# Kernel optimization log

Measured on AMD Instinct MI355X. Metric: run time of the kernel, lower is better.

The kernel has to match this reference:

```python
import jax, jax.numpy as jnp
import numpy as np


def setup_inputs() -> dict:
    key = jax.random.key(0)
    ks = jax.random.split(key, 6)
    B, S, H, I, E = 2, 1024, 1024, 2816, 8
    W = 0.02  # weight init scale
    return {
        "x": jax.random.normal(ks[0], (B, S, H), jnp.float32),
        "w_router": jax.random.normal(ks[1], (H, E), jnp.float32) * W,
        "w_gate": jax.random.normal(ks[2], (E, H, I), jnp.float32) * W,
        "w_up": jax.random.normal(ks[3], (E, H, I), jnp.float32) * W,
        "w_down": jax.random.normal(ks[4], (E, I, H), jnp.float32) * W,
        "b_down": jnp.zeros((E, H), jnp.float32),
    }


def reference(x, w_router, w_gate, w_up, w_down, b_down):
    # Eval path of PrunedLlamaSMoEBlock: noiseless router, top-k select, softmax
    # over selected logits, SwiGLU experts, scatter-add combine.
    NUM_SELECTS = 2
    T = x.shape[0] * x.shape[1]
    E = w_router.shape[1]
    flat_x = x.reshape(T, -1)                      # [T,H]

    logits = flat_x @ w_router                     # [T,E]
    top_vals, top_idx = jax.lax.top_k(logits, NUM_SELECTS)   # [T,k]
    gw = jax.nn.softmax(top_vals.astype(jnp.float32), axis=1).astype(x.dtype)

    # Dense combine weights: combine[t,e] = sum_k gw[t,k] * (top_idx[t,k]==e)
    combine = jnp.zeros((T, E), x.dtype).at[
        jnp.arange(T)[:, None], top_idx
    ].add(gw)                                      # [T,E]

    # SwiGLU experts over all tokens (weighted by combine, zero if unselected)
    g = jnp.einsum("th,ehi->tei", flat_x, w_gate)  # [T,E,I]
    u = jnp.einsum("th,ehi->tei", flat_x, w_up)    # [T,E,I]
    a = jax.nn.silu(g) * u                         # [T,E,I]
    y = jnp.einsum("tei,eih->teh", a, w_down) + b_down[None]  # [T,E,H]

    out = jnp.einsum("te,teh->th", combine, y)     # [T,H]
    return out.reshape(x.shape)
```

## Files before the change

kernel.cpp:

```cpp
#include <hip/hip_runtime.h>
#include <math.h>

#define HD __device__ __forceinline__

constexpr int TT = 2048;
constexpr int HH = 1024;
constexpr int II = 2816;
constexpr int EE = 8;
constexpr int NK1 = HH / 64;
constexpr int NK2 = II / 64;
constexpr int KS2 = 2;
constexpr int HALF2 = NK2 / KS2;
constexpr int MAXTILES = 40;
constexpr int NSLOT = 2 * TT;

typedef short  bf16x8  __attribute__((ext_vector_type(8)));
typedef float  floatx4 __attribute__((ext_vector_type(4)));
typedef unsigned short ushortx8 __attribute__((ext_vector_type(8)));

constexpr size_t OFF_XB    = 0;
constexpr size_t OFF_WGT   = OFF_XB    + (size_t)TT*HH*2;
constexpr size_t OFF_WUT   = OFF_WGT   + (size_t)EE*II*HH*2;
constexpr size_t OFF_WDT   = OFF_WUT   + (size_t)EE*II*HH*2;
constexpr size_t OFF_ABUF  = OFF_WDT   + (size_t)EE*HH*II*2;
constexpr size_t OFF_CNT   = OFF_ABUF  + (size_t)2*TT*II*2;
constexpr size_t OFF_OFFS  = OFF_CNT   + 256;
constexpr size_t OFF_MDESC = OFF_OFFS  + 256;
constexpr size_t OFF_EMETA = OFF_MDESC + 256;
constexpr size_t OFF_WMETA = OFF_EMETA + 16384;
constexpr size_t OFF_TLIST = OFF_WMETA + 16384;
constexpr size_t OFF_SLOT  = OFF_TLIST + 16384;
constexpr size_t OFF_YBUF  = OFF_WGT;

HD unsigned short f2bf(float f) {
  union { float f; unsigned int u; } v; v.f = f;
  return (unsigned short)((v.u + 0x7fffu + ((v.u >> 16) & 1u)) >> 16);
}

HD void load_lds16(const void* gptr, void* lptr) {
  __builtin_amdgcn_global_load_lds(
      (const __attribute__((address_space(1))) void*)gptr,
      (__attribute__((address_space(3))) void*)lptr,
      16, 0, 0);
}

__global__ __launch_bounds__(256)
void prep_router_kernel(const float* __restrict__ x, const float* __restrict__ w_router,
                        unsigned short* __restrict__ xb,
                        int* __restrict__ emeta, float* __restrict__ wmeta) {
  const int wave = threadIdx.x >> 6;
  const int lane = threadIdx.x & 63;
  const int t = blockIdx.x * 4 + wave;
  const float* xr = x + (size_t)t * HH;
  unsigned short* xo = xb + (size_t)t * HH;

  float acc[EE];
#pragma unroll
  for (int e = 0; e < EE; ++e) acc[e] = 0.f;

#pragma unroll
  for (int it = 0; it < 4; ++it) {
    const int h0 = it * 256 + lane * 4;
    const floatx4 v = __builtin_nontemporal_load((const floatx4*)(xr + h0));
    ushort4 o;
    o.x = f2bf(v[0]); o.y = f2bf(v[1]); o.z = f2bf(v[2]); o.w = f2bf(v[3]);
    *(ushort4*)(xo + h0) = o;
    const float vv[4] = {v[0], v[1], v[2], v[3]};
#pragma unroll
    for (int j = 0; j < 4; ++j) {
      const float* wr = w_router + (size_t)(h0 + j) * EE;
      const float4 w0 = ((const float4*)wr)[0];
      const float4 w1 = ((const float4*)wr)[1];
      acc[0] += vv[j] * w0.x; acc[1] += vv[j] * w0.y;
      acc[2] += vv[j] * w0.z; acc[3] += vv[j] * w0.w;
      acc[4] += vv[j] * w1.x; acc[5] += vv[j] * w1.y;
      acc[6] += vv[j] * w1.z; acc[7] += vv[j] * w1.w;
    }
  }
#pragma unroll
  for (int e = 0; e < EE; ++e) {
#pragma unroll
    for (int off = 32; off > 0; off >>= 1) acc[e] += __shfl_xor(acc[e], off, 64);
  }
  if (lane == 0) {
    int e0 = 0; float v0 = acc[0];
#pragma unroll
    for (int e = 1; e < EE; ++e) if (acc[e] > v0) { v0 = acc[e]; e0 = e; }
    int e1 = -1; float v1 = -3.4e38f;
#pragma unroll
    for (int e = 0; e < EE; ++e) if (e != e0 && acc[e] > v1) { v1 = acc[e]; e1 = e; }
    const float ex = __expf(v1 - v0);
    const float s  = 1.f + ex;
    emeta[2 * t] = e0; emeta[2 * t + 1] = e1;
    wmeta[2 * t] = 1.f / s; wmeta[2 * t + 1] = ex / s;
  }
}

__global__ __launch_bounds__(256)
void transpose_one_kernel(const float* __restrict__ src, unsigned short* __restrict__ dst,
                          int R, int C, int nct) {
  const int e = blockIdx.y;
  const int rt = blockIdx.x / nct;
  const int ct = blockIdx.x % nct;
  const size_t base = (size_t)e * R * C;
  const int R0 = rt * 64;
  const int C0 = ct * 128;

  const int lane = threadIdx.x & 63;
  const int wave = threadIdx.x >> 6;
  const int r0 = R0 + (lane & 7) * 8;
  const int c0 = C0 + wave * 32 + (lane >> 3) * 4;

  floatx4 v[8];
  const float* sp = src + base + (size_t)r0 * C + c0;
#pragma unroll
  for (int j = 0; j < 8; ++j)
    v[j] = __builtin_nontemporal_load((const floatx4*)(sp + (size_t)j * C));

  unsigned short* dp = dst + base + (size_t)c0 * R + r0;
#pragma unroll
  for (int jj = 0; jj < 4; ++jj) {
    ushortx8 o;
#pragma unroll
    for (int j = 0; j < 8; ++j) o[j] = f2bf(v[j][jj]);
    *(ushortx8*)(dp + (size_t)jj * R) = o;
  }
}

__global__ __launch_bounds__(256)
void scanfill_kernel(const int* __restrict__ emeta,
                     int* __restrict__ offsets, int* __restrict__ mdesc,
                     int* __restrict__ token_list, int* __restrict__ slotmap) {
  __shared__ int s_tot[EE];
  __shared__ int s_scan[256];
  const int e = blockIdx.x;
  const int tid = threadIdx.x;
  constexpr int CH = TT / 256;
  const int t0 = tid * CH;
  int lc[EE];
#pragma unroll
  for (int i = 0; i < EE; ++i) lc[i] = 0;
  int ep[CH][2];
#pragma unroll
  for (int k = 0; k < CH; ++k) {
    const int a = emeta[2 * (t0 + k)];
    const int b = emeta[2 * (t0 + k) + 1];
    ep[k][0] = a; ep[k][1] = b;
#pragma unroll
    for (int i = 0; i < EE; ++i) lc[i] += (a == i) + (b == i);
  }
  if (tid < EE) s_tot[tid] = 0;
  __syncthreads();
#pragma unroll
  for (int i = 0; i < EE; ++i) if (lc[i]) atomicAdd(&s_tot[i], lc[i]);
  int cnt = 0;
#pragma unroll
  for (int i = 0; i < EE; ++i) if (i == e) cnt = lc[i];
  s_scan[tid] = cnt;
  __syncthreads();
  int v = cnt;
  for (int d = 1; d < 256; d <<= 1) {
    const int add = (tid >= d) ? s_scan[tid - d] : 0;
    __syncthreads();
    v += add;
    s_scan[tid] = v;
    __syncthreads();
  }
  int off_e = 0;
#pragma unroll
  for (int i = 0; i < EE; ++i) off_e += (i < e) ? s_tot[i] : 0;
  if (e == 0 && tid == 0) {
    int s = 0, nt = 0;
    for (int i = 0; i < EE; ++i) {
      const int c = s_tot[i];
      offsets[i] = s;
      for (int m = 0; m < c; m += 128) mdesc[1 + nt++] = (i << 20) | m;
      s += c;
    }
    offsets[EE] = s;
    mdesc[0] = nt;
  }
  int pos = off_e + (v - cnt);
#pragma unroll
  for (int k = 0; k < CH; ++k) {
    const int t = t0 + k;
#pragma unroll
    for (int s = 0; s < 2; ++s) {
      if (ep[k][s] == e) {
        token_list[pos] = t;
        slotmap[2 * t + s] = pos;
        ++pos;
      }
    }
  }
}

__global__ __launch_bounds__(256, 4)
void gemm1_kernel(const unsigned short* __restrict__ xb,
                  const unsigned short* __restrict__ wgt,
                  const unsigned short* __restrict__ wut,
                  const int* __restrict__ offsets,
                  const int* __restrict__ mdesc,
                  const int* __restrict__ token_list,
                  unsigned short* __restrict__ Abuf) {
  constexpr int NWG1 = (II / 64) * MAXTILES;
  constexpr int CHUNK1 = NWG1 / 8;
  const int p = (int)(blockIdx.y * gridDim.x + blockIdx.x);
  const int idx = (p & 7) * CHUNK1 + (p >> 3);
  const int bx = idx / MAXTILES;
  const int by = idx % MAXTILES;

  if (by >= mdesc[0]) return;
  const int d = mdesc[1 + by];
  const int e = d >> 20;
  const int m_base = d & 0xFFFFF;
  const int off_e = offsets[e];
  const int n_e = offsets[e + 1] - off_e;
  const int n_base = bx * 64;

  __shared__ __attribute__((aligned(16))) unsigned short ldsA[128 * 64];
  __shared__ __attribute__((aligned(16))) unsigned short ldsG[64 * 64];
  __shared__ __attribute__((aligned(16))) unsigned short ldsU[64 * 64];

  const int tid = threadIdx.x;
  const int wave = tid >> 6;
  const int lane = tid & 63;
  const int quad = lane >> 4;
  const int l16 = lane & 15;
  const int wave_m = (wave & 1) * 64;
  const int wave_n = (wave >> 1) * 32;

  const int srow = lane >> 3;
  const int clog = (lane & 7) ^ srow;

  const unsigned short* gA[4];
  const unsigned short* gG[2];
  const unsigned short* gU[2];
#pragma unroll
  for (int it = 0; it < 4; ++it) {
    const int r = it * 32 + wave * 8 + srow;
    int ar = m_base + r; if (ar > n_e - 1) ar = n_e - 1;
    const int tok = token_list[off_e + ar];
    gA[it] = xb + (size_t)tok * HH + clog * 8;
  }
#pragma unroll
  for (int it = 0; it < 2; ++it) {
    const int r = it * 32 + wave * 8 + srow;
    gG[it] = wgt + ((size_t)e * II + (n_base + r)) * HH + clog * 8;
    gU[it] = wut + ((size_t)e * II + (n_base + r)) * HH + clog * 8;
  }

  floatx4 accG[4][2], accU[4][2];
  const floatx4 fz = {0.f, 0.f, 0.f, 0.f};
#pragma unroll
  for (int i = 0; i < 4; ++i)
#pragma unroll
    for (int j = 0; j < 2; ++j) { accG[i][j] = fz; accU[i][j] = fz; }

  for (int kt = 0; kt < NK1; ++kt) {
    const int k0 = kt * 64;
#pragma unroll
    for (int it = 0; it < 4; ++it)
      load_lds16(gA[it] + k0, &ldsA[(it * 32 + wave * 8) * 64]);
#pragma unroll
    for (int it = 0; it < 2; ++it) {
      load_lds16(gG[it] + k0, &ldsG[(it * 32 + wave * 8) * 64]);
      load_lds16(gU[it] + k0, &ldsU[(it * 32 + wave * 8) * 64]);
    }
    __syncthreads();
#pragma unroll
    for (int ks = 0; ks < 2; ++ks) {
      bf16x8 af[4], bg[2], bu[2];
#pragma unroll
      for (int f = 0; f < 4; ++f) {
        const int rowA = wave_m + f * 16 + l16;
        const int cA = (ks * 4 + quad) ^ (rowA & 7);
        af[f] = *(const bf16x8*)&ldsA[rowA * 64 + cA * 8];
      }
#pragma unroll
      for (int f = 0; f < 2; ++f) {
        const int rowB = wave_n + f * 16 + l16;
        const int cB = (ks * 4 + quad) ^ (rowB & 7);
        bg[f] = *(const bf16x8*)&ldsG[rowB * 64 + cB * 8];
        bu[f] = *(const bf16x8*)&ldsU[rowB * 64 + cB * 8];
      }
#pragma unroll
      for (int mf = 0; mf < 4; ++mf)
#pragma unroll
        for (int nf = 0; nf < 2; ++nf) {
          accG[mf][nf] = __builtin_amdgcn_mfma_f32_16x16x32_bf16(af[mf], bg[nf], accG[mf][nf], 0, 0, 0);
          accU[mf][nf] = __builtin_amdgcn_mfma_f32_16x16x32_bf16(af[mf], bu[nf], accU[mf][nf], 0, 0, 0);
        }
    }
    __syncthreads();
  }

#pragma unroll
  for (int mf = 0; mf < 4; ++mf)
#pragma unroll
    for (int nf = 0; nf < 2; ++nf) {
      const int col = n_base + wave_n + nf * 16 + l16;
#pragma unroll
      for (int j = 0; j < 4; ++j) {
        const int r = m_base + wave_m + mf * 16 + quad * 4 + j;
        if (r < n_e) {
          const float g = accG[mf][nf][j];
          const float u = accU[mf][nf][j];
          const float a = (g / (1.f + __expf(-g))) * u;
          Abuf[(size_t)(off_e + r) * II + col] = f2bf(a);
        }
      }
    }
}

__global__ __launch_bounds__(256, 3)
void gemm2_kernel(const unsigned short* __restrict__ Abuf,
                  const unsigned short* __restrict__ wdt,
                  const int* __restrict__ offsets,
                  const int* __restrict__ mdesc,
                  float* __restrict__ Ybuf) {
  const int p = (int)(blockIdx.x + gridDim.x * (blockIdx.y + gridDim.y * blockIdx.z));
  const int idx = (p & 7) * 80 + (p >> 3);
  const int by = idx % MAXTILES;
  const int g = idx / MAXTILES;
  const int bx = g & 7;
  const int split = g >> 3;

  if (by >= mdesc[0]) return;
  const int d = mdesc[1 + by];
  const int e = d >> 20;
  const int m_base = d & 0xFFFFF;
  const int off_e = offsets[e];
  const int n_e = offsets[e + 1] - off_e;
  const int n_base = bx * 128;
  const int kt_lo = split * HALF2;
  const int kt_hi = kt_lo + HALF2;

  __shared__ __attribute__((aligned(16))) unsigned short ldsA[128 * 64];
  __shared__ __attribute__((aligned(16))) unsigned short ldsB[128 * 64];

  const int tid = threadIdx.x;
  const int wave = tid >> 6;
  const int lane = tid & 63;
  const int quad = lane >> 4;
  const int l16 = lane & 15;
  const int wave_m = (wave & 1) * 64;
  const int wave_n = (wave >> 1) * 64;

  const int srow = lane >> 3;
  const int clog = (lane & 7) ^ srow;

  const unsigned short* gA[4];
  const unsigned short* gB[4];
#pragma unroll
  for (int it = 0; it < 4; ++it) {
    const int r = it * 32 + wave * 8 + srow;
    int ar = m_base + r; if (ar > n_e - 1) ar = n_e - 1;
    gA[it] = Abuf + (size_t)(off_e + ar) * II + clog * 8;
  }
#pragma unroll
  for (int it = 0; it < 4; ++it) {
    const int r = it * 32 + wave * 8 + srow;
    gB[it] = wdt + ((size_t)e * HH + (n_base + r)) * II + clog * 8;
  }

  floatx4 acc[4][4];
  const floatx4 fz = {0.f, 0.f, 0.f, 0.f};
#pragma unroll
  for (int i = 0; i < 4; ++i)
#pragma unroll
    for (int j = 0; j < 4; ++j) acc[i][j] = fz;

  for (int kt = kt_lo; kt < kt_hi; ++kt) {
    const int k0 = kt * 64;
#pragma unroll
    for (int it = 0; it < 4; ++it)
      load_lds16(gA[it] + k0, &ldsA[(it * 32 + wave * 8) * 64]);
#pragma unroll
    for (int it = 0; it < 4; ++it)
      load_lds16(gB[it] + k0, &ldsB[(it * 32 + wave * 8) * 64]);
    __syncthreads();
#pragma unroll
    for (int ks = 0; ks < 2; ++ks) {
      bf16x8 af[4], bf[4];
#pragma unroll
      for (int f = 0; f < 4; ++f) {
        const int rowA = wave_m + f * 16 + l16;
        const int cA = (ks * 4 + quad) ^ (rowA & 7);
        af[f] = *(const bf16x8*)&ldsA[rowA * 64 + cA * 8];
      }
#pragma unroll
      for (int f = 0; f < 4; ++f) {
        const int rowB = wave_n + f * 16 + l16;
        const int cB = (ks * 4 + quad) ^ (rowB & 7);
        bf[f] = *(const bf16x8*)&ldsB[rowB * 64 + cB * 8];
      }
#pragma unroll
      for (int mf = 0; mf < 4; ++mf)
#pragma unroll
        for (int nf = 0; nf < 4; ++nf)
          acc[mf][nf] = __builtin_amdgcn_mfma_f32_16x16x32_bf16(af[mf], bf[nf], acc[mf][nf], 0, 0, 0);
    }
    __syncthreads();
  }

  float* yb = Ybuf + (size_t)split * NSLOT * HH;
#pragma unroll
  for (int mf = 0; mf < 4; ++mf)
#pragma unroll
    for (int nf = 0; nf < 4; ++nf) {
      const int col = n_base + wave_n + nf * 16 + l16;
#pragma unroll
      for (int j = 0; j < 4; ++j) {
        const int r = m_base + wave_m + mf * 16 + quad * 4 + j;
        if (r < n_e)
          yb[(size_t)(off_e + r) * HH + col] = acc[mf][nf][j];
      }
    }
}

__global__ __launch_bounds__(256)
void combine_kernel(const float* __restrict__ Ybuf, const int* __restrict__ slotmap,
                    const int* __restrict__ emeta, const float* __restrict__ wmeta,
                    const float* __restrict__ b_down, float* __restrict__ out) {
  const int t = blockIdx.x;
  const int c = threadIdx.x;
  const int s0 = slotmap[2 * t], s1 = slotmap[2 * t + 1];
  const int e0 = emeta[2 * t], e1 = emeta[2 * t + 1];
  const float g0 = wmeta[2 * t], g1 = wmeta[2 * t + 1];
  const floatx4 y00 = __builtin_nontemporal_load((const floatx4*)(Ybuf + (size_t)s0 * HH) + c);
  const floatx4 y01 = __builtin_nontemporal_load((const floatx4*)(Ybuf + ((size_t)NSLOT + s0) * HH) + c);
  const floatx4 y10 = __builtin_nontemporal_load((const floatx4*)(Ybuf + (size_t)s1 * HH) + c);
  const floatx4 y11 = __builtin_nontemporal_load((const floatx4*)(Ybuf + ((size_t)NSLOT + s1) * HH) + c);
  const float4 b0 = ((const float4*)(b_down + (size_t)e0 * HH))[c];
  const float4 b1 = ((const float4*)(b_down + (size_t)e1 * HH))[c];
  float4 o;
  o.x = g0 * (y00[0] + y01[0] + b0.x) + g1 * (y10[0] + y11[0] + b1.x);
  o.y = g0 * (y00[1] + y01[1] + b0.y) + g1 * (y10[1] + y11[1] + b1.y);
  o.z = g0 * (y00[2] + y01[2] + b0.z) + g1 * (y10[2] + y11[2] + b1.z);
  o.w = g0 * (y00[3] + y01[3] + b0.w) + g1 * (y10[3] + y11[3] + b1.w);
  ((float4*)(out + (size_t)t * HH))[c] = o;
}

extern "C" void kernel_launch(void* const* d_in, const int* in_sizes, int n_in,
                              void* d_out, int out_size, void* d_ws, size_t ws_size,
                              hipStream_t stream) {
  const float* x        = (const float*)d_in[0];
  const float* w_router = (const float*)d_in[1];
  const float* w_gate   = (const float*)d_in[2];
  const float* w_up     = (const float*)d_in[3];
  const float* w_down   = (const float*)d_in[4];
  const float* b_down   = (const float*)d_in[5];
  float* out = (float*)d_out;

  char* ws = (char*)d_ws;
  unsigned short* xb   = (unsigned short*)(ws + OFF_XB);
  unsigned short* wgt  = (unsigned short*)(ws + OFF_WGT);
  unsigned short* wut  = (unsigned short*)(ws + OFF_WUT);
  unsigned short* wdt  = (unsigned short*)(ws + OFF_WDT);
  unsigned short* Abuf = (unsigned short*)(ws + OFF_ABUF);
  int*   offsets = (int*)(ws + OFF_OFFS);
  int*   mdesc   = (int*)(ws + OFF_MDESC);
  int*   emeta   = (int*)(ws + OFF_EMETA);
  float* wmeta   = (float*)(ws + OFF_WMETA);
  int*   tlist   = (int*)(ws + OFF_TLIST);
  int*   slotmap = (int*)(ws + OFF_SLOT);
  float* Ybuf    = (float*)(ws + OFF_YBUF);

  prep_router_kernel<<<TT / 4, 256, 0, stream>>>(x, w_router, xb, emeta, wmeta);
  scanfill_kernel<<<EE, 256, 0, stream>>>(emeta, offsets, mdesc, tlist, slotmap);
  transpose_one_kernel<<<dim3(352, EE), 256, 0, stream>>>(w_gate, wgt, HH, II, II / 128);
  transpose_one_kernel<<<dim3(352, EE), 256, 0, stream>>>(w_up,   wut, HH, II, II / 128);
  transpose_one_kernel<<<dim3(352, EE), 256, 0, stream>>>(w_down, wdt, II, HH, HH / 128);
  gemm1_kernel<<<dim3(II / 64, MAXTILES), 256, 0, stream>>>(xb, wgt, wut, offsets, mdesc, tlist, Abuf);
  gemm2_kernel<<<dim3(HH / 128, MAXTILES, KS2), 256, 0, stream>>>(Abuf, wdt, offsets, mdesc, Ybuf);
  combine_kernel<<<TT, 256, 0, stream>>>(Ybuf, slotmap, emeta, wmeta, b_down, out);
}
```

Before: 392.0 us.

## Merge prologue kernels and fuse combine into gemm2 via atomic scatter-add

Folds the router/convert kernel and the three weight transpose kernels into a single prologue launch, which also zeroes the output. It removes the combine kernel by having gemm2 scale each tile by its gate weight, add the bias on one split, and atomically add into the output rows indexed by the token list. This avoids the fp32 Y buffer round-trip and several launches, in exchange for many scattered fp32 atomics and a summation order that is no longer deterministic.

```diff
diff --git a/kernel.cpp b/kernel.cpp
--- a/kernel.cpp
+++ b/kernel.cpp
@@ -12,7 +12,6 @@
 constexpr int KS2 = 2;
 constexpr int HALF2 = NK2 / KS2;
 constexpr int MAXTILES = 40;
-constexpr int NSLOT = 2 * TT;
 
 typedef short  bf16x8  __attribute__((ext_vector_type(8)));
 typedef float  floatx4 __attribute__((ext_vector_type(4)));
@@ -23,14 +22,12 @@
 constexpr size_t OFF_WUT   = OFF_WGT   + (size_t)EE*II*HH*2;
 constexpr size_t OFF_WDT   = OFF_WUT   + (size_t)EE*II*HH*2;
 constexpr size_t OFF_ABUF  = OFF_WDT   + (size_t)EE*HH*II*2;
-constexpr size_t OFF_CNT   = OFF_ABUF  + (size_t)2*TT*II*2;
-constexpr size_t OFF_OFFS  = OFF_CNT   + 256;
+constexpr size_t OFF_OFFS  = OFF_ABUF  + (size_t)2*TT*II*2;
 constexpr size_t OFF_MDESC = OFF_OFFS  + 256;
 constexpr size_t OFF_EMETA = OFF_MDESC + 256;
 constexpr size_t OFF_WMETA = OFF_EMETA + 16384;
 constexpr size_t OFF_TLIST = OFF_WMETA + 16384;
-constexpr size_t OFF_SLOT  = OFF_TLIST + 16384;
-constexpr size_t OFF_YBUF  = OFF_WGT;
+constexpr size_t OFF_GWL   = OFF_TLIST + 16384;
 
 HD unsigned short f2bf(float f) {
   union { float f; unsigned int u; } v; v.f = f;
@@ -45,63 +42,77 @@
 }
 
 __global__ __launch_bounds__(256)
-void prep_router_kernel(const float* __restrict__ x, const float* __restrict__ w_router,
-                        unsigned short* __restrict__ xb,
-                        int* __restrict__ emeta, float* __restrict__ wmeta) {
-  const int wave = threadIdx.x >> 6;
-  const int lane = threadIdx.x & 63;
-  const int t = blockIdx.x * 4 + wave;
-  const float* xr = x + (size_t)t * HH;
-  unsigned short* xo = xb + (size_t)t * HH;
-
-  float acc[EE];
-#pragma unroll
-  for (int e = 0; e < EE; ++e) acc[e] = 0.f;
-
-#pragma unroll
-  for (int it = 0; it < 4; ++it) {
-    const int h0 = it * 256 + lane * 4;
-    const floatx4 v = __builtin_nontemporal_load((const floatx4*)(xr + h0));
-    ushort4 o;
-    o.x = f2bf(v[0]); o.y = f2bf(v[1]); o.z = f2bf(v[2]); o.w = f2bf(v[3]);
-    *(ushort4*)(xo + h0) = o;
-    const float vv[4] = {v[0], v[1], v[2], v[3]};
-#pragma unroll
-    for (int j = 0; j < 4; ++j) {
-      const float* wr = w_router + (size_t)(h0 + j) * EE;
-      const float4 w0 = ((const float4*)wr)[0];
-      const float4 w1 = ((const float4*)wr)[1];
-      acc[0] += vv[j] * w0.x; acc[1] += vv[j] * w0.y;
-      acc[2] += vv[j] * w0.z; acc[3] += vv[j] * w0.w;
-      acc[4] += vv[j] * w1.x; acc[5] += vv[j] * w1.y;
-      acc[6] += vv[j] * w1.z; acc[7] += vv[j] * w1.w;
-    }
-  }
-#pragma unroll
-  for (int e = 0; e < EE; ++e) {
-#pragma unroll
-    for (int off = 32; off > 0; off >>= 1) acc[e] += __shfl_xor(acc[e], off, 64);
-  }
-  if (lane == 0) {
-    int e0 = 0; float v0 = acc[0];
-#pragma unroll
-    for (int e = 1; e < EE; ++e) if (acc[e] > v0) { v0 = acc[e]; e0 = e; }
-    int e1 = -1; float v1 = -3.4e38f;
-#pragma unroll
-    for (int e = 0; e < EE; ++e) if (e != e0 && acc[e] > v1) { v1 = acc[e]; e1 = e; }
-    const float ex = __expf(v1 - v0);
-    const float s  = 1.f + ex;
-    emeta[2 * t] = e0; emeta[2 * t + 1] = e1;
-    wmeta[2 * t] = 1.f / s; wmeta[2 * t + 1] = ex / s;
-  }
-}
-
-__global__ __launch_bounds__(256)
-void transpose_one_kernel(const float* __restrict__ src, unsigned short* __restrict__ dst,
-                          int R, int C, int nct) {
-  const int e = blockIdx.y;
-  const int rt = blockIdx.x / nct;
-  const int ct = blockIdx.x % nct;
+void prologue_kernel(const float* __restrict__ x, const float* __restrict__ w_router,
+                     const float* __restrict__ wg, const float* __restrict__ wu,
+                     const float* __restrict__ wd,
+                     unsigned short* __restrict__ xb, int* __restrict__ emeta,
+                     float* __restrict__ wmeta, float* __restrict__ out,
+                     unsigned short* __restrict__ wgt, unsigned short* __restrict__ wut,
+                     unsigned short* __restrict__ wdt) {
+  const int ty = blockIdx.y;
+  if (ty == 0) {
+    if ((int)blockIdx.x >= TT / 4) return;
+    const int wave = threadIdx.x >> 6;
+    const int lane = threadIdx.x & 63;
+    const int t = blockIdx.x * 4 + wave;
+    const float* xr = x + (size_t)t * HH;
+    unsigned short* xo = xb + (size_t)t * HH;
+    float* orow = out + (size_t)t * HH;
+
+    float acc[EE];
+#pragma unroll
+    for (int e = 0; e < EE; ++e) acc[e] = 0.f;
+
+#pragma unroll
+    for (int it = 0; it < 4; ++it) {
+      const int h0 = it * 256 + lane * 4;
+      const floatx4 v = __builtin_nontemporal_load((const floatx4*)(xr + h0));
+      ushort4 o;
+      o.x = f2bf(v[0]); o.y = f2bf(v[1]); o.z = f2bf(v[2]); o.w = f2bf(v[3]);
+      *(ushort4*)(xo + h0) = o;
+      const float4 z = {0.f, 0.f, 0.f, 0.f};
+      *(float4*)(orow + h0) = z;
+      const float vv[4] = {v[0], v[1], v[2], v[3]};
+#pragma unroll
+      for (int j = 0; j < 4; ++j) {
+        const float* wr = w_router + (size_t)(h0 + j) * EE;
+        const float4 w0 = ((const float4*)wr)[0];
+        const float4 w1 = ((const float4*)wr)[1];
+        acc[0] += vv[j] * w0.x; acc[1] += vv[j] * w0.y;
+        acc[2] += vv[j] * w0.z; acc[3] += vv[j] * w0.w;
+        acc[4] += vv[j] * w1.x; acc[5] += vv[j] * w1.y;
+        acc[6] += vv[j] * w1.z; acc[7] += vv[j] * w1.w;
+      }
+    }
+#pragma unroll
+    for (int e = 0; e < EE; ++e) {
+#pragma unroll
+      for (int off = 32; off > 0; off >>= 1) acc[e] += __shfl_xor(acc[e], off, 64);
+    }
+    if (lane == 0) {
+      int e0 = 0; float v0 = acc[0];
+#pragma unroll
+      for (int e = 1; e < EE; ++e) if (acc[e] > v0) { v0 = acc[e]; e0 = e; }
+      int e1 = -1; float v1 = -3.4e38f;
+#pragma unroll
+      for (int e = 0; e < EE; ++e) if (e != e0 && acc[e] > v1) { v1 = acc[e]; e1 = e; }
+      const float ex = __expf(v1 - v0);
+      const float s  = 1.f + ex;
+      emeta[2 * t] = e0; emeta[2 * t + 1] = e1;
+      wmeta[2 * t] = 1.f / s; wmeta[2 * t + 1] = ex / s;
+    }
+    return;
+  }
+
+  const float* src; unsigned short* dst; int R, C;
+  if (ty == 1)      { src = wg; dst = wgt; R = HH; C = II; }
+  else if (ty == 2) { src = wu; dst = wut; R = HH; C = II; }
+  else              { src = wd; dst = wdt; R = II; C = HH; }
+  const int e = blockIdx.x / 352;
+  const int tile = blockIdx.x % 352;
+  const int nct = C / 128;
+  const int rt = tile / nct;
+  const int ct = tile % nct;
   const size_t base = (size_t)e * R * C;
   const int R0 = rt * 64;
   const int C0 = ct * 128;
@@ -128,9 +139,9 @@
 }
 
 __global__ __launch_bounds__(256)
-void scanfill_kernel(const int* __restrict__ emeta,
+void scanfill_kernel(const int* __restrict__ emeta, const float* __restrict__ wmeta,
                      int* __restrict__ offsets, int* __restrict__ mdesc,
-                     int* __restrict__ token_list, int* __restrict__ slotmap) {
+                     int* __restrict__ token_list, float* __restrict__ gw_list) {
   __shared__ int s_tot[EE];
   __shared__ int s_scan[256];
   const int e = blockIdx.x;
@@ -188,7 +199,7 @@
     for (int s = 0; s < 2; ++s) {
       if (ep[k][s] == e) {
         token_list[pos] = t;
-        slotmap[2 * t + s] = pos;
+        gw_list[pos] = wmeta[2 * t + s];
         ++pos;
       }
     }
@@ -316,9 +327,12 @@
 __global__ __launch_bounds__(256, 3)
 void gemm2_kernel(const unsigned short* __restrict__ Abuf,
                   const unsigned short* __restrict__ wdt,
+                  const float* __restrict__ b_down,
                   const int* __restrict__ offsets,
                   const int* __restrict__ mdesc,
-                  float* __restrict__ Ybuf) {
+                  const int* __restrict__ token_list,
+                  const float* __restrict__ gw_list,
+                  float* __restrict__ out) {
   const int p = (int)(blockIdx.x + gridDim.x * (blockIdx.y + gridDim.y * blockIdx.z));
   const int idx = (p & 7) * 80 + (p >> 3);
   const int by = idx % MAXTILES;
@@ -404,42 +418,22 @@
     __syncthreads();
   }
 
-  float* yb = Ybuf + (size_t)split * NSLOT * HH;
 #pragma unroll
   for (int mf = 0; mf < 4; ++mf)
 #pragma unroll
     for (int nf = 0; nf < 4; ++nf) {
       const int col = n_base + wave_n + nf * 16 + l16;
+      const float bd = (split == 0) ? b_down[e * HH + col] : 0.f;
 #pragma unroll
       for (int j = 0; j < 4; ++j) {
         const int r = m_base + wave_m + mf * 16 + quad * 4 + j;
-        if (r < n_e)
-          yb[(size_t)(off_e + r) * HH + col] = acc[mf][nf][j];
-      }
-    }
-}
-
-__global__ __launch_bounds__(256)
-void combine_kernel(const float* __restrict__ Ybuf, const int* __restrict__ slotmap,
-                    const int* __restrict__ emeta, const float* __restrict__ wmeta,
-                    const float* __restrict__ b_down, float* __restrict__ out) {
-  const int t = blockIdx.x;
-  const int c = threadIdx.x;
-  const int s0 = slotmap[2 * t], s1 = slotmap[2 * t + 1];
-  const int e0 = emeta[2 * t], e1 = emeta[2 * t + 1];
-  const float g0 = wmeta[2 * t], g1 = wmeta[2 * t + 1];
-  const floatx4 y00 = __builtin_nontemporal_load((const floatx4*)(Ybuf + (size_t)s0 * HH) + c);
-  const floatx4 y01 = __builtin_nontemporal_load((const floatx4*)(Ybuf + ((size_t)NSLOT + s0) * HH) + c);
-  const floatx4 y10 = __builtin_nontemporal_load((const floatx4*)(Ybuf + (size_t)s1 * HH) + c);
-  const floatx4 y11 = __builtin_nontemporal_load((const floatx4*)(Ybuf + ((size_t)NSLOT + s1) * HH) + c);
-  const float4 b0 = ((const float4*)(b_down + (size_t)e0 * HH))[c];
-  const float4 b1 = ((const float4*)(b_down + (size_t)e1 * HH))[c];
-  float4 o;
-  o.x = g0 * (y00[0] + y01[0] + b0.x) + g1 * (y10[0] + y11[0] + b1.x);
-  o.y = g0 * (y00[1] + y01[1] + b0.y) + g1 * (y10[1] + y11[1] + b1.y);
-  o.z = g0 * (y00[2] + y01[2] + b0.z) + g1 * (y10[2] + y11[2] + b1.z);
-  o.w = g0 * (y00[3] + y01[3] + b0.w) + g1 * (y10[3] + y11[3] + b1.w);
-  ((float4*)(out + (size_t)t * HH))[c] = o;
+        if (r < n_e) {
+          const int cr = off_e + r;
+          atomicAdd(&out[(size_t)token_list[cr] * HH + col],
+                    gw_list[cr] * (acc[mf][nf][j] + bd));
+        }
+      }
+    }
 }
 
 extern "C" void kernel_launch(void* const* d_in, const int* in_sizes, int n_in,
@@ -464,15 +458,12 @@
   int*   emeta   = (int*)(ws + OFF_EMETA);
   float* wmeta   = (float*)(ws + OFF_WMETA);
   int*   tlist   = (int*)(ws + OFF_TLIST);
-  int*   slotmap = (int*)(ws + OFF_SLOT);
-  float* Ybuf    = (float*)(ws + OFF_YBUF);
-
-  prep_router_kernel<<<TT / 4, 256, 0, stream>>>(x, w_router, xb, emeta, wmeta);
-  scanfill_kernel<<<EE, 256, 0, stream>>>(emeta, offsets, mdesc, tlist, slotmap);
-  transpose_one_kernel<<<dim3(352, EE), 256, 0, stream>>>(w_gate, wgt, HH, II, II / 128);
-  transpose_one_kernel<<<dim3(352, EE), 256, 0, stream>>>(w_up,   wut, HH, II, II / 128);
-  transpose_one_kernel<<<dim3(352, EE), 256, 0, stream>>>(w_down, wdt, II, HH, HH / 128);
+  float* gwl     = (float*)(ws + OFF_GWL);
+
+  prologue_kernel<<<dim3(352 * EE, 4), 256, 0, stream>>>(
+      x, w_router, w_gate, w_up, w_down, xb, emeta, wmeta, out, wgt, wut, wdt);
+  scanfill_kernel<<<EE, 256, 0, stream>>>(emeta, wmeta, offsets, mdesc, tlist, gwl);
   gemm1_kernel<<<dim3(II / 64, MAXTILES), 256, 0, stream>>>(xb, wgt, wut, offsets, mdesc, tlist, Abuf);
-  gemm2_kernel<<<dim3(HH / 128, MAXTILES, KS2), 256, 0, stream>>>(Abuf, wdt, offsets, mdesc, Ybuf);
-  combine_kernel<<<TT, 256, 0, stream>>>(Ybuf, slotmap, emeta, wmeta, b_down, out);
-}
+  gemm2_kernel<<<dim3(HH / 128, MAXTILES, KS2), 256, 0, stream>>>(
+      Abuf, wdt, b_down, offsets, mdesc, tlist, gwl, out);
+}
```

New measurement: 407.3 us. +3.9%, slower.

## Fuse router prep and three weight transposes into one prologue kernel

Applied to the files above, without the earlier changes.

Merges the router/bf16-cast kernel and the three weight transpose-and-convert launches into a single prologue kernel that uses grid y to select the job. This removes three launches and lets the router work overlap with the transposes. The transpose tile changes from 64x128 to 32x256, so each lane now reads wider contiguous rows. Gemm1's launch bounds go from 4 to 5 waves per SIMD, which could limit registers and cause spills. An unused workspace offset is also dropped.

```diff
diff --git a/kernel.cpp b/kernel.cpp
--- a/kernel.cpp
+++ b/kernel.cpp
@@ -23,8 +23,7 @@
 constexpr size_t OFF_WUT   = OFF_WGT   + (size_t)EE*II*HH*2;
 constexpr size_t OFF_WDT   = OFF_WUT   + (size_t)EE*II*HH*2;
 constexpr size_t OFF_ABUF  = OFF_WDT   + (size_t)EE*HH*II*2;
-constexpr size_t OFF_CNT   = OFF_ABUF  + (size_t)2*TT*II*2;
-constexpr size_t OFF_OFFS  = OFF_CNT   + 256;
+constexpr size_t OFF_OFFS  = OFF_ABUF  + (size_t)2*TT*II*2;
 constexpr size_t OFF_MDESC = OFF_OFFS  + 256;
 constexpr size_t OFF_EMETA = OFF_MDESC + 256;
 constexpr size_t OFF_WMETA = OFF_EMETA + 16384;
@@ -45,71 +44,83 @@
 }
 
 __global__ __launch_bounds__(256)
-void prep_router_kernel(const float* __restrict__ x, const float* __restrict__ w_router,
-                        unsigned short* __restrict__ xb,
-                        int* __restrict__ emeta, float* __restrict__ wmeta) {
-  const int wave = threadIdx.x >> 6;
-  const int lane = threadIdx.x & 63;
-  const int t = blockIdx.x * 4 + wave;
-  const float* xr = x + (size_t)t * HH;
-  unsigned short* xo = xb + (size_t)t * HH;
-
-  float acc[EE];
-#pragma unroll
-  for (int e = 0; e < EE; ++e) acc[e] = 0.f;
-
-#pragma unroll
-  for (int it = 0; it < 4; ++it) {
-    const int h0 = it * 256 + lane * 4;
-    const floatx4 v = __builtin_nontemporal_load((const floatx4*)(xr + h0));
-    ushort4 o;
-    o.x = f2bf(v[0]); o.y = f2bf(v[1]); o.z = f2bf(v[2]); o.w = f2bf(v[3]);
-    *(ushort4*)(xo + h0) = o;
-    const float vv[4] = {v[0], v[1], v[2], v[3]};
-#pragma unroll
-    for (int j = 0; j < 4; ++j) {
-      const float* wr = w_router + (size_t)(h0 + j) * EE;
-      const float4 w0 = ((const float4*)wr)[0];
-      const float4 w1 = ((const float4*)wr)[1];
-      acc[0] += vv[j] * w0.x; acc[1] += vv[j] * w0.y;
-      acc[2] += vv[j] * w0.z; acc[3] += vv[j] * w0.w;
-      acc[4] += vv[j] * w1.x; acc[5] += vv[j] * w1.y;
-      acc[6] += vv[j] * w1.z; acc[7] += vv[j] * w1.w;
-    }
-  }
-#pragma unroll
-  for (int e = 0; e < EE; ++e) {
-#pragma unroll
-    for (int off = 32; off > 0; off >>= 1) acc[e] += __shfl_xor(acc[e], off, 64);
-  }
-  if (lane == 0) {
-    int e0 = 0; float v0 = acc[0];
-#pragma unroll
-    for (int e = 1; e < EE; ++e) if (acc[e] > v0) { v0 = acc[e]; e0 = e; }
-    int e1 = -1; float v1 = -3.4e38f;
-#pragma unroll
-    for (int e = 0; e < EE; ++e) if (e != e0 && acc[e] > v1) { v1 = acc[e]; e1 = e; }
-    const float ex = __expf(v1 - v0);
-    const float s  = 1.f + ex;
-    emeta[2 * t] = e0; emeta[2 * t + 1] = e1;
-    wmeta[2 * t] = 1.f / s; wmeta[2 * t + 1] = ex / s;
-  }
-}
-
-__global__ __launch_bounds__(256)
-void transpose_one_kernel(const float* __restrict__ src, unsigned short* __restrict__ dst,
-                          int R, int C, int nct) {
-  const int e = blockIdx.y;
-  const int rt = blockIdx.x / nct;
-  const int ct = blockIdx.x % nct;
+void prologue_kernel(const float* __restrict__ x, const float* __restrict__ w_router,
+                     const float* __restrict__ wg, const float* __restrict__ wu,
+                     const float* __restrict__ wd,
+                     unsigned short* __restrict__ xb, int* __restrict__ emeta,
+                     float* __restrict__ wmeta,
+                     unsigned short* __restrict__ wgt, unsigned short* __restrict__ wut,
+                     unsigned short* __restrict__ wdt) {
+  const int ty = blockIdx.y;
+  if (ty == 0) {
+    if ((int)blockIdx.x >= TT / 4) return;
+    const int wave = threadIdx.x >> 6;
+    const int lane = threadIdx.x & 63;
+    const int t = blockIdx.x * 4 + wave;
+    const float* xr = x + (size_t)t * HH;
+    unsigned short* xo = xb + (size_t)t * HH;
+
+    float acc[EE];
+#pragma unroll
+    for (int e = 0; e < EE; ++e) acc[e] = 0.f;
+
+#pragma unroll
+    for (int it = 0; it < 4; ++it) {
+      const int h0 = it * 256 + lane * 4;
+      const floatx4 v = __builtin_nontemporal_load((const floatx4*)(xr + h0));
+      ushort4 o;
+      o.x = f2bf(v[0]); o.y = f2bf(v[1]); o.z = f2bf(v[2]); o.w = f2bf(v[3]);
+      *(ushort4*)(xo + h0) = o;
+      const float vv[4] = {v[0], v[1], v[2], v[3]};
+#pragma unroll
+      for (int j = 0; j < 4; ++j) {
+        const float* wr = w_router + (size_t)(h0 + j) * EE;
+        const float4 w0 = ((const float4*)wr)[0];
+        const float4 w1 = ((const float4*)wr)[1];
+        acc[0] += vv[j] * w0.x; acc[1] += vv[j] * w0.y;
+        acc[2] += vv[j] * w0.z; acc[3] += vv[j] * w0.w;
+        acc[4] += vv[j] * w1.x; acc[5] += vv[j] * w1.y;
+        acc[6] += vv[j] * w1.z; acc[7] += vv[j] * w1.w;
+      }
+    }
+#pragma unroll
+    for (int e = 0; e < EE; ++e) {
+#pragma unroll
+      for (int off = 32; off > 0; off >>= 1) acc[e] += __shfl_xor(acc[e], off, 64);
+    }
+    if (lane == 0) {
+      int e0 = 0; float v0 = acc[0];
+#pragma unroll
+      for (int e = 1; e < EE; ++e) if (acc[e] > v0) { v0 = acc[e]; e0 = e; }
+      int e1 = -1; float v1 = -3.4e38f;
+#pragma unroll
+      for (int e = 0; e < EE; ++e) if (e != e0 && acc[e] > v1) { v1 = acc[e]; e1 = e; }
+      const float ex = __expf(v1 - v0);
+      const float s  = 1.f + ex;
+      emeta[2 * t] = e0; emeta[2 * t + 1] = e1;
+      wmeta[2 * t] = 1.f / s; wmeta[2 * t + 1] = ex / s;
+    }
+    return;
+  }
+
+  const float* src; unsigned short* dst; int R, C, nct;
+  if (ty == 1)      { src = wg; dst = wgt; R = HH; C = II; nct = II / 256; }
+  else if (ty == 2) { src = wu; dst = wut; R = HH; C = II; nct = II / 256; }
+  else              { src = wd; dst = wdt; R = II; C = HH; nct = HH / 256; }
+  const int e = blockIdx.x / 352;
+  const int tile = blockIdx.x % 352;
+  const int rt = tile / nct;
+  const int ct = tile % nct;
   const size_t base = (size_t)e * R * C;
-  const int R0 = rt * 64;
-  const int C0 = ct * 128;
+  const int R0 = rt * 32;
+  const int C0 = ct * 256;
 
   const int lane = threadIdx.x & 63;
   const int wave = threadIdx.x >> 6;
-  const int r0 = R0 + (lane & 7) * 8;
-  const int c0 = C0 + wave * 32 + (lane >> 3) * 4;
+  const int rowgrp = lane >> 4;
+  const int colchunk = lane & 15;
+  const int r0 = R0 + rowgrp * 8;
+  const int c0 = C0 + wave * 64 + colchunk * 4;
 
   floatx4 v[8];
   const float* sp = src + base + (size_t)r0 * C + c0;
@@ -195,7 +206,7 @@
   }
 }
 
-__global__ __launch_bounds__(256, 4)
+__global__ __launch_bounds__(256, 5)
 void gemm1_kernel(const unsigned short* __restrict__ xb,
                   const unsigned short* __restrict__ wgt,
                   const unsigned short* __restrict__ wut,
@@ -467,11 +478,9 @@
   int*   slotmap = (int*)(ws + OFF_SLOT);
   float* Ybuf    = (float*)(ws + OFF_YBUF);
 
-  prep_router_kernel<<<TT / 4, 256, 0, stream>>>(x, w_router, xb, emeta, wmeta);
+  prologue_kernel<<<dim3(352 * EE, 4), 256, 0, stream>>>(
+      x, w_router, w_gate, w_up, w_down, xb, emeta, wmeta, wgt, wut, wdt);
   scanfill_kernel<<<EE, 256, 0, stream>>>(emeta, offsets, mdesc, tlist, slotmap);
-  transpose_one_kernel<<<dim3(352, EE), 256, 0, stream>>>(w_gate, wgt, HH, II, II / 128);
-  transpose_one_kernel<<<dim3(352, EE), 256, 0, stream>>>(w_up,   wut, HH, II, II / 128);
-  transpose_one_kernel<<<dim3(352, EE), 256, 0, stream>>>(w_down, wdt, II, HH, HH / 128);
   gemm1_kernel<<<dim3(II / 64, MAXTILES), 256, 0, stream>>>(xb, wgt, wut, offsets, mdesc, tlist, Abuf);
   gemm2_kernel<<<dim3(HH / 128, MAXTILES, KS2), 256, 0, stream>>>(Abuf, wdt, offsets, mdesc, Ybuf);
   combine_kernel<<<TT, 256, 0, stream>>>(Ybuf, slotmap, emeta, wmeta, b_down, out);
```

Measured after the change: 434.6 us. 10.9% more time.
